# Kernel optimization log

Hardware: AMD Instinct MI355X
Metric: run time of the kernel (lower is better)

The kernel has to match this reference:

```python
import jax, jax.numpy as jnp
import numpy as np

N = 65536      # total nodes = B * MAXN
E = 524288     # edges (avg degree 8)
DX = 32; DG = 32
IN_DIM = DX + 3 * DG   # 128, after concat(x, g0, g1, g2)
H = 256; OUT = 8; MAXN = 8192


def setup_inputs() -> dict:
    key = jax.random.key(0)
    ks = jax.random.split(key, 40)
    inp = {}
    inp['x'] = jax.random.normal(ks[0], (N, DX), jnp.float32)
    inp['g0'] = jax.random.normal(ks[1], (N, DG), jnp.float32)
    inp['g1'] = jax.random.normal(ks[2], (N, DG), jnp.float32)
    inp['g2'] = jax.random.normal(ks[3], (N, DG), jnp.float32)
    inp['edge_src'] = jax.random.randint(ks[4], (E,), 0, N, jnp.int32)
    inp['edge_dst'] = jax.random.randint(ks[5], (E,), 0, N, jnp.int32)
    dims = [(IN_DIM, H), (H, H), (H, H), (H, H)]
    k = 6
    for i, (di, do) in enumerate(dims):
        s = 1.0 / np.sqrt(di)
        inp[f'Wl{i}'] = jax.random.uniform(ks[k], (di, do), jnp.float32, -s, s); k += 1
        inp[f'Wr{i}'] = jax.random.uniform(ks[k], (di, do), jnp.float32, -s, s); k += 1
        inp[f'b{i}'] = jnp.zeros((do,), jnp.float32)
    s = 1.0 / np.sqrt(MAXN)
    inp['mlp1_W1'] = jax.random.uniform(ks[k], (MAXN, H), jnp.float32, -s, s); k += 1
    inp['mlp1_b1'] = jnp.zeros((H,), jnp.float32)
    s = 1.0 / np.sqrt(H)
    inp['mlp1_W2'] = jax.random.uniform(ks[k], (H, 1), jnp.float32, -s, s); k += 1
    inp['mlp1_b2'] = jnp.zeros((1,), jnp.float32)
    inp['bn_gamma'] = jnp.ones((H,), jnp.float32)
    inp['bn_beta'] = jnp.zeros((H,), jnp.float32)
    inp['mlp2_W1'] = jax.random.uniform(ks[k], (H, H), jnp.float32, -s, s); k += 1
    inp['mlp2_b1'] = jnp.zeros((H,), jnp.float32)
    inp['mlp2_W2'] = jax.random.uniform(ks[k], (H, OUT), jnp.float32, -s, s); k += 1
    inp['mlp2_b2'] = jnp.zeros((OUT,), jnp.float32)
    return inp


def _forward(x, g0, g1, g2, edge_src, edge_dst,
             Wl0, Wr0, b0, Wl1, Wr1, b1, Wl2, Wr2, b2, Wl3, Wr3, b3,
             mlp1_W1, mlp1_b1, mlp1_W2, mlp1_b2, bn_gamma, bn_beta,
             mlp2_W1, mlp2_b1, mlp2_W2, mlp2_b2):
    h = jnp.concatenate([x, g0, g1, g2], axis=1)  # [N, IN_DIM]
    # mean-aggregation denominator (in-degree, clamped at 1 like PyG mean)
    cnt = jnp.maximum(
        jax.ops.segment_sum(jnp.ones((E,), h.dtype), edge_dst, num_segments=N), 1.0)
    for Wl, Wr, b in ((Wl0, Wr0, b0), (Wl1, Wr1, b1), (Wl2, Wr2, b2), (Wl3, Wr3, b3)):
        agg = jax.ops.segment_sum(h[edge_src], edge_dst, num_segments=N) / cnt[:, None]
        # SAGEConv: lin_l(mean of neighbors) + lin_r(self) + bias, then ReLU
        h = jax.nn.relu(agg @ Wl + h @ Wr + b)
        # F.dropout in eval / deterministic reference: identity
    h = h.reshape(-1, H, MAXN)                               # [B, H, MAXN]
    h = jax.nn.relu(jnp.einsum('bhm,mk->bhk', h, mlp1_W1) + mlp1_b1)
    h = (jnp.einsum('bhk,ko->bho', h, mlp1_W2) + mlp1_b2)[..., 0]  # [B, H]
    mean = h.mean(axis=0)
    var = h.var(axis=0)
    h = (h - mean) / jnp.sqrt(var + 1e-5) * bn_gamma + bn_beta
    h = jax.nn.relu(h)
    h = jax.nn.relu(h @ mlp2_W1 + mlp2_b1)
    return h @ mlp2_W2 + mlp2_b2                              # [B, OUT]


def reference(x, g0, g1, g2, edge_src, edge_dst,
              Wl0, Wr0, b0, Wl1, Wr1, b1, Wl2, Wr2, b2, Wl3, Wr3, b3,
              mlp1_W1, mlp1_b1, mlp1_W2, mlp1_b2, bn_gamma, bn_beta,
              mlp2_W1, mlp2_b1, mlp2_W2, mlp2_b2):
    return _forward(x, g0, g1, g2, edge_src, edge_dst,
                    Wl0, Wr0, b0, Wl1, Wr1, b1, Wl2, Wr2, b2, Wl3, Wr3, b3,
                    mlp1_W1, mlp1_b1, mlp1_W2, mlp1_b2, bn_gamma, bn_beta,
                    mlp2_W1, mlp2_b1, mlp2_W2, mlp2_b2)
```

## Files before the change

kernel.cpp:

```cpp
#include <hip/hip_runtime.h>
#include <hip/hip_bf16.h>


#define NN 65536
#define EE 524288
#define ROWS 65537
#define PCSR_CAP 983040

using frag16 = __attribute__((ext_vector_type(8))) short;
using f32x4  = __attribute__((ext_vector_type(4))) float;
using us8    = __attribute__((ext_vector_type(8))) unsigned short;
using us4v   = __attribute__((ext_vector_type(4))) unsigned short;

__device__ __forceinline__ float b2f(unsigned short u) {
    union { unsigned u32; float f; } x; x.u32 = (unsigned)u << 16; return x.f;
}

__device__ __forceinline__ void gld_lds16(const void* g, void* l) {
    __builtin_amdgcn_global_load_lds(
        (const __attribute__((address_space(1))) void*)g,
        (__attribute__((address_space(3))) void*)l, 16, 0, 0);
}

struct B1Args {
    const float* tsrc[9];
    __hip_bfloat16* tdst[9];
    int ldk[9];
    int kofs[9];
    int kblk[9];
    const float *x, *g0, *g1, *g2;
    __hip_bfloat16* h;
    int* ideg;
};

__global__ void gs_batch1(B1Args a) {
    const int z = blockIdx.z;
    const int t = threadIdx.x;
    __shared__ float tile[32][33];
    if (z == 0) {
        if (blockIdx.y != 0) return;
        int i = blockIdx.x * 256 + t;
        if (i < NN) a.ideg[i] = 0;
        return;
    }
    if (z <= 9) {
        const int m = z - 1;
        if ((int)blockIdx.x >= a.kblk[m]) return;
        const float* src = a.tsrc[m];
        __hip_bfloat16* dst = a.tdst[m];
        int ldk = a.ldk[m], kofs = a.kofs[m];
        int kb = blockIdx.x * 32, nb = blockIdx.y * 32;
        int tx = t & 31, ty = t >> 5;
#pragma unroll
        for (int i2 = 0; i2 < 32; i2 += 8)
            tile[ty + i2][tx] = src[(size_t)(kb + ty + i2) * 256 + nb + tx];
        __syncthreads();
#pragma unroll
        for (int i2 = 0; i2 < 32; i2 += 8) {
            int n = nb + ty + i2, k = kb + tx;
            dst[(size_t)n * ldk + kofs + k] = __float2bfloat16(tile[tx][ty + i2]);
        }
        return;
    }
    int vb0 = blockIdx.y * 256 + blockIdx.x;
#pragma unroll
    for (int s = 0; s < 4; ++s) {
        int idx = (s * 2048 + vb0) * 256 + t;
        int n = idx >> 5, q = idx & 31;
        int c0 = q * 4;
        const float* src = (c0 < 32) ? (a.x  + (size_t)n * 32 + c0)
                         : (c0 < 64) ? (a.g0 + (size_t)n * 32 + (c0 - 32))
                         : (c0 < 96) ? (a.g1 + (size_t)n * 32 + (c0 - 64))
                                     : (a.g2 + (size_t)n * 32 + (c0 - 96));
        f32x4 v = *(const f32x4*)src;
        union { us4v u; __hip_bfloat16 b[4]; } o;
#pragma unroll
        for (int r = 0; r < 4; ++r) o.b[r] = __float2bfloat16(v[r]);
        *(us4v*)(a.h + (size_t)n * 512 + 256 + c0) = o.u;
    }
}


__global__ void gs_hist(const int* __restrict__ dst, int* __restrict__ deg) {
    int e = blockIdx.x * 256 + threadIdx.x;
    atomicAdd(&deg[dst[e]], 1);
}

__global__ void gs_deg_reduce(const int* __restrict__ deg, int* __restrict__ bsum) {
    int t = threadIdx.x;
    int p = (deg[blockIdx.x * 256 + t] + 7) & ~7;
#pragma unroll
    for (int off = 32; off > 0; off >>= 1) p += __shfl_down(p, off);
    __shared__ int w4[4];
    if ((t & 63) == 0) w4[t >> 6] = p;
    __syncthreads();
    if (t == 0) bsum[blockIdx.x] = w4[0] + w4[1] + w4[2] + w4[3];
}

__global__ void gs_scan_apply(const int* __restrict__ deg, const int* __restrict__ bsum,
                              int* __restrict__ prow, int* __restrict__ cursor,
                              float* __restrict__ inv_cnt, int* __restrict__ pcsr,
                              __hip_bfloat16* __restrict__ P0,
                              __hip_bfloat16* __restrict__ P1) {
    __shared__ int part[256];
    int t = threadIdx.x;
    part[t] = bsum[t];
    __syncthreads();
    for (int off = 1; off < 256; off <<= 1) {
        int add = (t >= off) ? part[t - off] : 0;
        __syncthreads();
        part[t] += add;
        __syncthreads();
    }
    int blk_ofs = part[blockIdx.x] - bsum[blockIdx.x];
    int total = part[255];
    __syncthreads();
    int i = blockIdx.x * 256 + t;
    int d = deg[i];
    int p = (d + 7) & ~7;
    part[t] = p;
    __syncthreads();
    for (int off = 1; off < 256; off <<= 1) {
        int add = (t >= off) ? part[t - off] : 0;
        __syncthreads();
        part[t] += add;
        __syncthreads();
    }
    int beg = blk_ofs + part[t] - p;
    prow[i] = beg;
    cursor[i] = beg;
    inv_cnt[i] = 1.0f / (float)(d > 0 ? d : 1);
    for (int j = d; j < p; ++j) pcsr[beg + j] = NN;
    if (i == NN - 1) prow[NN] = total;
    if (blockIdx.x == 0) {
        ((unsigned*)(P0 + (size_t)NN * 512))[t] = 0u;
        ((unsigned*)(P1 + (size_t)NN * 512))[t] = 0u;
    }
}

__global__ void gs_bucket(const int* __restrict__ src, const int* __restrict__ dst,
                          int* __restrict__ cursor, int* __restrict__ pcsr) {
    int e = blockIdx.x * 256 + threadIdx.x;
    int d = dst[e];
    int p = atomicAdd(&cursor[d], 1);
    pcsr[p] = src[e];
}

template <int DIM>
__global__ void gs_agg_bf(const __hip_bfloat16* __restrict__ hsrc,
                          __hip_bfloat16* __restrict__ adst,
                          const int* __restrict__ prow, const int* __restrict__ pcsr,
                          const float* __restrict__ inv_cnt) {
    constexpr int EL = DIM / 32;
    int wave = threadIdx.x >> 6;
    int lane = threadIdx.x & 63;
    int n = blockIdx.x * 4 + wave;
    int e = prow[n], pe = prow[n + 1];
    float iv = inv_cnt[n];
    const int half = lane >> 5;
    const __hip_bfloat16* base = hsrc + (lane & 31) * EL;
    float a[EL];
#pragma unroll
    for (int k = 0; k < EL; ++k) a[k] = 0.f;
    int4 sa, sb;
    if (e < pe) { sa = *(const int4*)(pcsr + e); sb = *(const int4*)(pcsr + e + 4); }
    while (e < pe) {
        int4 ca = sa, cb = sb;
        e += 8;
        if (e < pe) { sa = *(const int4*)(pcsr + e); sb = *(const int4*)(pcsr + e + 4); }
        int r0 = half ? ca.y : ca.x;
        int r1 = half ? ca.w : ca.z;
        int r2 = half ? cb.y : cb.x;
        int r3 = half ? cb.w : cb.z;
        if constexpr (DIM == 256) {
            us8 v0 = *(const us8*)(base + (size_t)r0 * 512);
            us8 v1 = *(const us8*)(base + (size_t)r1 * 512);
            us8 v2 = *(const us8*)(base + (size_t)r2 * 512);
            us8 v3 = *(const us8*)(base + (size_t)r3 * 512);
#pragma unroll
            for (int k = 0; k < 8; ++k)
                a[k] += b2f(v0[k]) + b2f(v1[k]) + b2f(v2[k]) + b2f(v3[k]);
        } else {
            us4v v0 = *(const us4v*)(base + (size_t)r0 * 512);
            us4v v1 = *(const us4v*)(base + (size_t)r1 * 512);
            us4v v2 = *(const us4v*)(base + (size_t)r2 * 512);
            us4v v3 = *(const us4v*)(base + (size_t)r3 * 512);
#pragma unroll
            for (int k = 0; k < 4; ++k)
                a[k] += b2f(v0[k]) + b2f(v1[k]) + b2f(v2[k]) + b2f(v3[k]);
        }
    }
#pragma unroll
    for (int k = 0; k < EL; ++k) a[k] += __shfl_xor(a[k], 32);
    if (half == 0) {
        union { us8 v8; us4v v4; __hip_bfloat16 b[8]; } o;
#pragma unroll
        for (int k = 0; k < EL; ++k) o.b[k] = __float2bfloat16(a[k] * iv);
        if constexpr (DIM == 256)
            *(us8*)(adst + (size_t)n * 512 + (lane & 31) * 8) = o.v8;
        else
            *(us4v*)(adst + (size_t)n * 512 + (lane & 31) * 4) = o.v4;
    }
}


__device__ __forceinline__ void stage_tile256(const __hip_bfloat16* __restrict__ A, int lda,
                                              const __hip_bfloat16* __restrict__ Bt, int ldb,
                                              size_t row0, int kc,
                                              __hip_bfloat16* As, __hip_bfloat16* Bs) {
    const int t = threadIdx.x;
#pragma unroll
    for (int l = 0; l < 4; ++l) {
        int c = l * 512 + t;
        int row = c >> 3;
        int col = ((c & 7) ^ (row & 7)) * 8;
        gld_lds16(A + (row0 + row) * (size_t)lda + kc + col, As + c * 8);
        gld_lds16(Bt + (size_t)row * ldb + kc + col, Bs + c * 8);
    }
}

__device__ __forceinline__ void compute_tile256(const __hip_bfloat16* As,
                                                const __hip_bfloat16* Bs,
                                                int wm, int wn, int ml, int cq,
                                                f32x4 (&acc)[8][4]) {
#pragma unroll
    for (int kk = 0; kk < 2; ++kk) {
        const int g = kk * 4 + cq;
        frag16 a[8], b[4];
#pragma unroll
        for (int i = 0; i < 8; ++i) {
            int row = wm * 128 + i * 16 + ml;
            a[i] = *(const frag16*)(As + row * 64 + ((g ^ (row & 7)) * 8));
        }
#pragma unroll
        for (int j = 0; j < 4; ++j) {
            int row = wn * 64 + j * 16 + ml;
            b[j] = *(const frag16*)(Bs + row * 64 + ((g ^ (row & 7)) * 8));
        }
        __builtin_amdgcn_s_setprio(1);
#pragma unroll
        for (int i = 0; i < 8; ++i)
#pragma unroll
            for (int j = 0; j < 4; ++j)
                acc[i][j] = __builtin_amdgcn_mfma_f32_16x16x32_bf16(b[j], a[i], acc[i][j], 0, 0, 0);
        __builtin_amdgcn_s_setprio(0);
    }
}

__device__ __forceinline__ void gemm256_loop(const __hip_bfloat16* __restrict__ A, int lda,
                                             const __hip_bfloat16* __restrict__ Bt, int ldb,
                                             size_t row0, int kbeg, int nt,
                                             __hip_bfloat16 (&As)[2][256 * 64],
                                             __hip_bfloat16 (&Bs)[2][256 * 64],
                                             int wm, int wn, int ml, int cq,
                                             f32x4 (&acc)[8][4]) {
    stage_tile256(A, lda, Bt, ldb, row0, kbeg, As[0], Bs[0]);
    int cur = 0;
    for (int kt = 0; kt < nt; ++kt) {
        if (kt + 1 < nt) {
            stage_tile256(A, lda, Bt, ldb, row0, kbeg + (kt + 1) * 64, As[cur ^ 1], Bs[cur ^ 1]);
            asm volatile("s_waitcnt vmcnt(8)" ::: "memory");
        } else {
            asm volatile("s_waitcnt vmcnt(0)" ::: "memory");
        }
        asm volatile("s_barrier" ::: "memory");
        compute_tile256(As[cur], Bs[cur], wm, wn, ml, cq, acc);
        asm volatile("s_barrier" ::: "memory");
        cur ^= 1;
    }
}

__global__ __launch_bounds__(512, 2)
void gs_gemm8_bias_relu(const __hip_bfloat16* __restrict__ A, int lda, int K,
                        const __hip_bfloat16* __restrict__ Bt, int ldb,
                        const float* __restrict__ bias,
                        __hip_bfloat16* __restrict__ C, int ldc, int cofs) {
    __shared__ __hip_bfloat16 As[2][256 * 64];
    __shared__ __hip_bfloat16 Bs[2][256 * 64];
    f32x4 acc[8][4] = {};
    const size_t row0 = (size_t)blockIdx.x * 256;
    const int lane = threadIdx.x & 63, wid = threadIdx.x >> 6;
    const int wm = wid >> 2, wn = wid & 3, ml = lane & 15, cq = lane >> 4;
    gemm256_loop(A, lda, Bt, ldb, row0, 0, K / 64, As, Bs, wm, wn, ml, cq, acc);
#pragma unroll
    for (int i = 0; i < 8; ++i) {
        size_t row = row0 + wm * 128 + i * 16 + ml;
#pragma unroll
        for (int j = 0; j < 4; ++j) {
            int n0 = wn * 64 + j * 16 + cq * 4;
            f32x4 bv = *(const f32x4*)(bias + n0);
            union { us4v v; __hip_bfloat16 b[4]; } o;
#pragma unroll
            for (int r = 0; r < 4; ++r)
                o.b[r] = __float2bfloat16(fmaxf(acc[i][j][r] + bv[r], 0.f));
            *(us4v*)(C + row * (size_t)ldc + cofs + n0) = o.v;
        }
    }
}

__global__ __launch_bounds__(512, 2)
void gs_gemm8_splitk(const __hip_bfloat16* __restrict__ A, int lda,
                     const __hip_bfloat16* __restrict__ Bt, int ldb,
                     float* __restrict__ part) {
    __shared__ __hip_bfloat16 As[2][256 * 64];
    __shared__ __hip_bfloat16 Bs[2][256 * 64];
    f32x4 acc[8][4] = {};
    const size_t row0 = (size_t)blockIdx.x * 256;
    const int kbeg = blockIdx.y * 512;
    const int lane = threadIdx.x & 63, wid = threadIdx.x >> 6;
    const int wm = wid >> 2, wn = wid & 3, ml = lane & 15, cq = lane >> 4;
    gemm256_loop(A, lda, Bt, ldb, row0, kbeg, 8, As, Bs, wm, wn, ml, cq, acc);
    float* p = part + (size_t)blockIdx.y * 2048 * 256;
#pragma unroll
    for (int i = 0; i < 8; ++i) {
        size_t row = row0 + wm * 128 + i * 16 + ml;
#pragma unroll
        for (int j = 0; j < 4; ++j) {
            int n0 = wn * 64 + j * 16 + cq * 4;
            *(f32x4*)(p + row * 256 + n0) = acc[i][j];
        }
    }
}

__global__ void gs_mlp1_pool(const float* __restrict__ part, const float* __restrict__ b1,
                             const float* __restrict__ W2, const float* __restrict__ b2,
                             float* __restrict__ pooled) {
    int r = blockIdx.x;
    int t = threadIdx.x;
    float s = 0.f;
#pragma unroll
    for (int ks = 0; ks < 16; ++ks) s += part[(size_t)ks * 524288 + r * 256 + t];
    s = fmaxf(s + b1[t], 0.f) * W2[t];
#pragma unroll
    for (int off = 32; off > 0; off >>= 1) s += __shfl_down(s, off);
    __shared__ float w4[4];
    if ((t & 63) == 0) w4[t >> 6] = s;
    __syncthreads();
    if (t == 0) pooled[r] = w4[0] + w4[1] + w4[2] + w4[3] + b2[0];
}

__global__ void gs_bn_mlp2(const float* __restrict__ pooled, const float* __restrict__ gamma,
                           const float* __restrict__ beta, const float* __restrict__ W1,
                           const float* __restrict__ b1, const float* __restrict__ W2,
                           const float* __restrict__ b2, float* __restrict__ out) {
    __shared__ float hb[8][256];
    __shared__ float h2[8][256];
    int t = threadIdx.x;
    {
        float v[8];
        float m = 0.f;
#pragma unroll
        for (int b = 0; b < 8; ++b) { v[b] = pooled[b * 256 + t]; m += v[b]; }
        m *= 0.125f;
        float var = 0.f;
#pragma unroll
        for (int b = 0; b < 8; ++b) { float d = v[b] - m; var += d * d; }
        var *= 0.125f;
        float is = 1.0f / sqrtf(var + 1e-5f);
        float g = gamma[t], bt = beta[t];
#pragma unroll
        for (int b = 0; b < 8; ++b) hb[b][t] = fmaxf((v[b] - m) * is * g + bt, 0.f);
    }
    __syncthreads();
    {
        float acc[8] = {};
        for (int i = 0; i < 256; ++i) {
            float w = W1[i * 256 + t];
#pragma unroll
            for (int b = 0; b < 8; ++b) acc[b] = fmaf(hb[b][i], w, acc[b]);
        }
        float bb = b1[t];
#pragma unroll
        for (int b = 0; b < 8; ++b) h2[b][t] = fmaxf(acc[b] + bb, 0.f);
    }
    __syncthreads();
    if (t < 64) {
        int b = t >> 3, o = t & 7;
        float acc = 0.f;
        for (int j = 0; j < 256; ++j) acc = fmaf(h2[b][j], W2[j * 8 + o], acc);
        out[b * 8 + o] = acc + b2[o];
    }
}

extern "C" void kernel_launch(void* const* d_in, const int* in_sizes, int n_in,
                              void* d_out, int out_size, void* d_ws, size_t ws_size,
                              hipStream_t stream) {
    const float* x  = (const float*)d_in[0];
    const float* g0 = (const float*)d_in[1];
    const float* g1 = (const float*)d_in[2];
    const float* g2 = (const float*)d_in[3];
    const int* edge_src = (const int*)d_in[4];
    const int* edge_dst = (const int*)d_in[5];
    const float* Wl[4] = {(const float*)d_in[6], (const float*)d_in[9],
                          (const float*)d_in[12], (const float*)d_in[15]};
    const float* Wr[4] = {(const float*)d_in[7], (const float*)d_in[10],
                          (const float*)d_in[13], (const float*)d_in[16]};
    const float* bs[4] = {(const float*)d_in[8], (const float*)d_in[11],
                          (const float*)d_in[14], (const float*)d_in[17]};
    const float* mlp1_W1 = (const float*)d_in[18];
    const float* mlp1_b1 = (const float*)d_in[19];
    const float* mlp1_W2 = (const float*)d_in[20];
    const float* mlp1_b2 = (const float*)d_in[21];
    const float* bn_gamma = (const float*)d_in[22];
    const float* bn_beta  = (const float*)d_in[23];
    const float* mlp2_W1 = (const float*)d_in[24];
    const float* mlp2_b1 = (const float*)d_in[25];
    const float* mlp2_W2 = (const float*)d_in[26];
    const float* mlp2_b2 = (const float*)d_in[27];
    float* out = (float*)d_out;

    char* ws = (char*)d_ws;
    __hip_bfloat16* P0 = (__hip_bfloat16*)ws;
    __hip_bfloat16* P1 = P0 + (size_t)ROWS * 512;
    __hip_bfloat16* WC0 = P1 + (size_t)ROWS * 512;
    __hip_bfloat16* WC1 = WC0 + 65536;
    __hip_bfloat16* WC2 = WC1 + 131072;
    __hip_bfloat16* WC3 = WC2 + 131072;
    __hip_bfloat16* W1T = WC3 + 131072;
    float* inv_cnt = (float*)(W1T + 2097152);
    int* ideg = (int*)(inv_cnt + 65536);
    int* prow = ideg + 65536;
    int* cursor = prow + 65544;
    int* bsum = cursor + 65536;
    int* pcsr = bsum + 256;
    __hip_bfloat16* H4 = P0;
    float* pooled = (float*)P1 + 524288;
    float* PART = (float*)((char*)P1 + (size_t)(4 << 20));

    {
        B1Args a;
        const float* srcs[9] = {Wl[0], Wr[0], Wl[1], Wr[1], Wl[2], Wr[2], Wl[3], Wr[3],
                                mlp1_W1};
        __hip_bfloat16* dsts[9] = {WC0, WC0, WC1, WC1, WC2, WC2, WC3, WC3, W1T};
        int ldks[9] = {256, 256, 512, 512, 512, 512, 512, 512, 8192};
        int kofss[9] = {0, 128, 0, 256, 0, 256, 0, 256, 0};
        int kblks[9] = {4, 4, 8, 8, 8, 8, 8, 8, 256};
        for (int i = 0; i < 9; ++i) {
            a.tsrc[i] = srcs[i]; a.tdst[i] = dsts[i];
            a.ldk[i] = ldks[i]; a.kofs[i] = kofss[i]; a.kblk[i] = kblks[i];
        }
        a.x = x; a.g0 = g0; a.g1 = g1; a.g2 = g2;
        a.h = P0; a.ideg = ideg;
        gs_batch1<<<dim3(256, 8, 11), 256, 0, stream>>>(a);
    }

    gs_hist<<<EE / 256, 256, 0, stream>>>(edge_dst, ideg);
    gs_deg_reduce<<<256, 256, 0, stream>>>(ideg, bsum);
    gs_scan_apply<<<256, 256, 0, stream>>>(ideg, bsum, prow, cursor, inv_cnt, pcsr, P0, P1);
    gs_bucket<<<EE / 256, 256, 0, stream>>>(edge_src, edge_dst, cursor, pcsr);

    gs_agg_bf<128><<<NN / 4, 256, 0, stream>>>(P0 + 256, P0 + 128, prow, pcsr, inv_cnt);
    gs_gemm8_bias_relu<<<NN / 256, 512, 0, stream>>>(P0 + 128, 512, 256, WC0, 256,
                                                     bs[0], P1, 512, 256);
    gs_agg_bf<256><<<NN / 4, 256, 0, stream>>>(P1 + 256, P1, prow, pcsr, inv_cnt);
    gs_gemm8_bias_relu<<<NN / 256, 512, 0, stream>>>(P1, 512, 512, WC1, 512,
                                                     bs[1], P0, 512, 256);
    gs_agg_bf<256><<<NN / 4, 256, 0, stream>>>(P0 + 256, P0, prow, pcsr, inv_cnt);
    gs_gemm8_bias_relu<<<NN / 256, 512, 0, stream>>>(P0, 512, 512, WC2, 512,
                                                     bs[2], P1, 512, 256);
    gs_agg_bf<256><<<NN / 4, 256, 0, stream>>>(P1 + 256, P1, prow, pcsr, inv_cnt);
    gs_gemm8_bias_relu<<<NN / 256, 512, 0, stream>>>(P1, 512, 512, WC3, 512,
                                                     bs[3], H4, 256, 0);

    gs_gemm8_splitk<<<dim3(2048 / 256, 16), 512, 0, stream>>>(H4, 8192, W1T, 8192, PART);
    gs_mlp1_pool<<<2048, 256, 0, stream>>>(PART, mlp1_b1, mlp1_W2, mlp1_b2, pooled);

    gs_bn_mlp2<<<1, 256, 0, stream>>>(pooled, bn_gamma, bn_beta, mlp2_W1, mlp2_b1,
                                      mlp2_W2, mlp2_b2, out);
}
```

Measured before the change: 520.1 us.

## Fuse neighbor aggregation into SAGE layer GEMM kernel per 256-row tile

Merges the gather-mean aggregation kernel into the GEMM kernel: each 512-thread block first aggregates neighbor features for its own 256 rows (each wave processes 32 nodes serially), then syncs and runs the bias+ReLU GEMM on those rows. This removes four kernel launches and lets the aggregated rows be reread while possibly still in cache. In exchange, aggregation now runs with only 256 blocks at 2 blocks/CU occupancy, with long serial per-wave loops, so there is less memory-level parallelism for the random gathers than the previous 16384-block launch had. There is also no overlap between the gather phase and the MFMA phase inside a block.

```diff
diff --git a/kernel.cpp b/kernel.cpp
--- a/kernel.cpp
+++ b/kernel.cpp
@@ -144,63 +144,6 @@
     int d = dst[e];
     int p = atomicAdd(&cursor[d], 1);
     pcsr[p] = src[e];
-}
-
-template <int DIM>
-__global__ void gs_agg_bf(const __hip_bfloat16* __restrict__ hsrc,
-                          __hip_bfloat16* __restrict__ adst,
-                          const int* __restrict__ prow, const int* __restrict__ pcsr,
-                          const float* __restrict__ inv_cnt) {
-    constexpr int EL = DIM / 32;
-    int wave = threadIdx.x >> 6;
-    int lane = threadIdx.x & 63;
-    int n = blockIdx.x * 4 + wave;
-    int e = prow[n], pe = prow[n + 1];
-    float iv = inv_cnt[n];
-    const int half = lane >> 5;
-    const __hip_bfloat16* base = hsrc + (lane & 31) * EL;
-    float a[EL];
-#pragma unroll
-    for (int k = 0; k < EL; ++k) a[k] = 0.f;
-    int4 sa, sb;
-    if (e < pe) { sa = *(const int4*)(pcsr + e); sb = *(const int4*)(pcsr + e + 4); }
-    while (e < pe) {
-        int4 ca = sa, cb = sb;
-        e += 8;
-        if (e < pe) { sa = *(const int4*)(pcsr + e); sb = *(const int4*)(pcsr + e + 4); }
-        int r0 = half ? ca.y : ca.x;
-        int r1 = half ? ca.w : ca.z;
-        int r2 = half ? cb.y : cb.x;
-        int r3 = half ? cb.w : cb.z;
-        if constexpr (DIM == 256) {
-            us8 v0 = *(const us8*)(base + (size_t)r0 * 512);
-            us8 v1 = *(const us8*)(base + (size_t)r1 * 512);
-            us8 v2 = *(const us8*)(base + (size_t)r2 * 512);
-            us8 v3 = *(const us8*)(base + (size_t)r3 * 512);
-#pragma unroll
-            for (int k = 0; k < 8; ++k)
-                a[k] += b2f(v0[k]) + b2f(v1[k]) + b2f(v2[k]) + b2f(v3[k]);
-        } else {
-            us4v v0 = *(const us4v*)(base + (size_t)r0 * 512);
-            us4v v1 = *(const us4v*)(base + (size_t)r1 * 512);
-            us4v v2 = *(const us4v*)(base + (size_t)r2 * 512);
-            us4v v3 = *(const us4v*)(base + (size_t)r3 * 512);
-#pragma unroll
-            for (int k = 0; k < 4; ++k)
-                a[k] += b2f(v0[k]) + b2f(v1[k]) + b2f(v2[k]) + b2f(v3[k]);
-        }
-    }
-#pragma unroll
-    for (int k = 0; k < EL; ++k) a[k] += __shfl_xor(a[k], 32);
-    if (half == 0) {
-        union { us8 v8; us4v v4; __hip_bfloat16 b[8]; } o;
-#pragma unroll
-        for (int k = 0; k < EL; ++k) o.b[k] = __float2bfloat16(a[k] * iv);
-        if constexpr (DIM == 256)
-            *(us8*)(adst + (size_t)n * 512 + (lane & 31) * 8) = o.v8;
-        else
-            *(us4v*)(adst + (size_t)n * 512 + (lane & 31) * 4) = o.v4;
-    }
 }
 
 
@@ -270,16 +213,78 @@
     }
 }
 
+template <int DIM>
 __global__ __launch_bounds__(512, 2)
-void gs_gemm8_bias_relu(const __hip_bfloat16* __restrict__ A, int lda, int K,
-                        const __hip_bfloat16* __restrict__ Bt, int ldb,
-                        const float* __restrict__ bias,
-                        __hip_bfloat16* __restrict__ C, int ldc, int cofs) {
+void gs_sage_layer(const __hip_bfloat16* __restrict__ hsrc,
+                   __hip_bfloat16* __restrict__ adst,
+                   const int* __restrict__ prow, const int* __restrict__ pcsr,
+                   const float* __restrict__ inv_cnt,
+                   const __hip_bfloat16* __restrict__ A, int lda, int K,
+                   const __hip_bfloat16* __restrict__ Bt, int ldb,
+                   const float* __restrict__ bias,
+                   __hip_bfloat16* __restrict__ C, int ldc, int cofs) {
     __shared__ __hip_bfloat16 As[2][256 * 64];
     __shared__ __hip_bfloat16 Bs[2][256 * 64];
+    const int lane = threadIdx.x & 63, wid = threadIdx.x >> 6;
+
+    {
+        constexpr int EL = DIM / 32;
+        const int half = lane >> 5;
+        const __hip_bfloat16* base = hsrc + (lane & 31) * EL;
+        const int n0 = blockIdx.x * 256 + wid * 32;
+        for (int u = 0; u < 32; ++u) {
+            int n = n0 + u;
+            int e = prow[n], pe = prow[n + 1];
+            float iv = inv_cnt[n];
+            float a[EL];
+#pragma unroll
+            for (int k = 0; k < EL; ++k) a[k] = 0.f;
+            int4 sa, sb;
+            if (e < pe) { sa = *(const int4*)(pcsr + e); sb = *(const int4*)(pcsr + e + 4); }
+            while (e < pe) {
+                int4 ca = sa, cb = sb;
+                e += 8;
+                if (e < pe) { sa = *(const int4*)(pcsr + e); sb = *(const int4*)(pcsr + e + 4); }
+                int r0 = half ? ca.y : ca.x;
+                int r1 = half ? ca.w : ca.z;
+                int r2 = half ? cb.y : cb.x;
+                int r3 = half ? cb.w : cb.z;
+                if constexpr (DIM == 256) {
+                    us8 v0 = *(const us8*)(base + (size_t)r0 * 512);
+                    us8 v1 = *(const us8*)(base + (size_t)r1 * 512);
+                    us8 v2 = *(const us8*)(base + (size_t)r2 * 512);
+                    us8 v3 = *(const us8*)(base + (size_t)r3 * 512);
+#pragma unroll
+                    for (int k = 0; k < 8; ++k)
+                        a[k] += b2f(v0[k]) + b2f(v1[k]) + b2f(v2[k]) + b2f(v3[k]);
+                } else {
+                    us4v v0 = *(const us4v*)(base + (size_t)r0 * 512);
+                    us4v v1 = *(const us4v*)(base + (size_t)r1 * 512);
+                    us4v v2 = *(const us4v*)(base + (size_t)r2 * 512);
+                    us4v v3 = *(const us4v*)(base + (size_t)r3 * 512);
+#pragma unroll
+                    for (int k = 0; k < 4; ++k)
+                        a[k] += b2f(v0[k]) + b2f(v1[k]) + b2f(v2[k]) + b2f(v3[k]);
+                }
+            }
+#pragma unroll
+            for (int k = 0; k < EL; ++k) a[k] += __shfl_xor(a[k], 32);
+            if (half == 0) {
+                union { us8 v8; us4v v4; __hip_bfloat16 b[8]; } o;
+#pragma unroll
+                for (int k = 0; k < EL; ++k) o.b[k] = __float2bfloat16(a[k] * iv);
+                if constexpr (DIM == 256)
+                    *(us8*)(adst + (size_t)n * 512 + (lane & 31) * 8) = o.v8;
+                else
+                    *(us4v*)(adst + (size_t)n * 512 + (lane & 31) * 4) = o.v4;
+            }
+        }
+    }
+    asm volatile("s_waitcnt vmcnt(0)" ::: "memory");
+    __syncthreads();
+
     f32x4 acc[8][4] = {};
     const size_t row0 = (size_t)blockIdx.x * 256;
-    const int lane = threadIdx.x & 63, wid = threadIdx.x >> 6;
     const int wm = wid >> 2, wn = wid & 3, ml = lane & 15, cq = lane >> 4;
     gemm256_loop(A, lda, Bt, ldb, row0, 0, K / 64, As, Bs, wm, wn, ml, cq, acc);
 #pragma unroll
@@ -449,18 +454,18 @@
     gs_scan_apply<<<256, 256, 0, stream>>>(ideg, bsum, prow, cursor, inv_cnt, pcsr, P0, P1);
     gs_bucket<<<EE / 256, 256, 0, stream>>>(edge_src, edge_dst, cursor, pcsr);
 
-    gs_agg_bf<128><<<NN / 4, 256, 0, stream>>>(P0 + 256, P0 + 128, prow, pcsr, inv_cnt);
-    gs_gemm8_bias_relu<<<NN / 256, 512, 0, stream>>>(P0 + 128, 512, 256, WC0, 256,
-                                                     bs[0], P1, 512, 256);
-    gs_agg_bf<256><<<NN / 4, 256, 0, stream>>>(P1 + 256, P1, prow, pcsr, inv_cnt);
-    gs_gemm8_bias_relu<<<NN / 256, 512, 0, stream>>>(P1, 512, 512, WC1, 512,
-                                                     bs[1], P0, 512, 256);
-    gs_agg_bf<256><<<NN / 4, 256, 0, stream>>>(P0 + 256, P0, prow, pcsr, inv_cnt);
-    gs_gemm8_bias_relu<<<NN / 256, 512, 0, stream>>>(P0, 512, 512, WC2, 512,
-                                                     bs[2], P1, 512, 256);
-    gs_agg_bf<256><<<NN / 4, 256, 0, stream>>>(P1 + 256, P1, prow, pcsr, inv_cnt);
-    gs_gemm8_bias_relu<<<NN / 256, 512, 0, stream>>>(P1, 512, 512, WC3, 512,
-                                                     bs[3], H4, 256, 0);
+    gs_sage_layer<128><<<NN / 256, 512, 0, stream>>>(
+        P0 + 256, P0 + 128, prow, pcsr, inv_cnt,
+        P0 + 128, 512, 256, WC0, 256, bs[0], P1, 512, 256);
+    gs_sage_layer<256><<<NN / 256, 512, 0, stream>>>(
+        P1 + 256, P1, prow, pcsr, inv_cnt,
+        P1, 512, 512, WC1, 512, bs[1], P0, 512, 256);
+    gs_sage_layer<256><<<NN / 256, 512, 0, stream>>>(
+        P0 + 256, P0, prow, pcsr, inv_cnt,
+        P0, 512, 512, WC2, 512, bs[2], P1, 512, 256);
+    gs_sage_layer<256><<<NN / 256, 512, 0, stream>>>(
+        P1 + 256, P1, prow, pcsr, inv_cnt,
+        P1, 512, 512, WC3, 512, bs[3], H4, 256, 0);
 
     gs_gemm8_splitk<<<dim3(2048 / 256, 16), 512, 0, stream>>>(H4, 8192, W1T, 8192, PART);
     gs_mlp1_pool<<<2048, 256, 0, stream>>>(PART, mlp1_b1, mlp1_W2, mlp1_b2, pooled);
```

After: 564.2 us. 8.5% more time.

## Pad CSR rows to 4 and use full-wave gathers in aggregation

Applied to the files above, without the earlier changes.

The neighbour padding granularity in the CSR drops from 8 to 4, so there are fewer dummy padding edges. The aggregation kernel changes from split half-waves, each handling half the neighbours with wider loads, to a full 64-lane wave that covers the whole feature row with narrower per-lane loads, processing 4 neighbours per iteration. This removes the cross-half shuffle reduction and the gathers wasted on padding, but each lane now issues narrower memory requests.

```diff
diff --git a/kernel.cpp b/kernel.cpp
--- a/kernel.cpp
+++ b/kernel.cpp
@@ -5,11 +5,10 @@
 #define NN 65536
 #define EE 524288
 #define ROWS 65537
-#define PCSR_CAP 983040
+#define PCSR_CAP 720896
 
 using frag16 = __attribute__((ext_vector_type(8))) short;
 using f32x4  = __attribute__((ext_vector_type(4))) float;
-using us8    = __attribute__((ext_vector_type(8))) unsigned short;
 using us4v   = __attribute__((ext_vector_type(4))) unsigned short;
 
 __device__ __forceinline__ float b2f(unsigned short u) {
@@ -88,7 +87,7 @@
 
 __global__ void gs_deg_reduce(const int* __restrict__ deg, int* __restrict__ bsum) {
     int t = threadIdx.x;
-    int p = (deg[blockIdx.x * 256 + t] + 7) & ~7;
+    int p = (deg[blockIdx.x * 256 + t] + 3) & ~3;
 #pragma unroll
     for (int off = 32; off > 0; off >>= 1) p += __shfl_down(p, off);
     __shared__ int w4[4];
@@ -117,7 +116,7 @@
     __syncthreads();
     int i = blockIdx.x * 256 + t;
     int d = deg[i];
-    int p = (d + 7) & ~7;
+    int p = (d + 3) & ~3;
     part[t] = p;
     __syncthreads();
     for (int off = 1; off < 256; off <<= 1) {
@@ -151,55 +150,52 @@
                           __hip_bfloat16* __restrict__ adst,
                           const int* __restrict__ prow, const int* __restrict__ pcsr,
                           const float* __restrict__ inv_cnt) {
-    constexpr int EL = DIM / 32;
     int wave = threadIdx.x >> 6;
     int lane = threadIdx.x & 63;
     int n = blockIdx.x * 4 + wave;
     int e = prow[n], pe = prow[n + 1];
     float iv = inv_cnt[n];
-    const int half = lane >> 5;
-    const __hip_bfloat16* base = hsrc + (lane & 31) * EL;
-    float a[EL];
-#pragma unroll
-    for (int k = 0; k < EL; ++k) a[k] = 0.f;
-    int4 sa, sb;
-    if (e < pe) { sa = *(const int4*)(pcsr + e); sb = *(const int4*)(pcsr + e + 4); }
-    while (e < pe) {
-        int4 ca = sa, cb = sb;
-        e += 8;
-        if (e < pe) { sa = *(const int4*)(pcsr + e); sb = *(const int4*)(pcsr + e + 4); }
-        int r0 = half ? ca.y : ca.x;
-        int r1 = half ? ca.w : ca.z;
-        int r2 = half ? cb.y : cb.x;
-        int r3 = half ? cb.w : cb.z;
-        if constexpr (DIM == 256) {
-            us8 v0 = *(const us8*)(base + (size_t)r0 * 512);
-            us8 v1 = *(const us8*)(base + (size_t)r1 * 512);
-            us8 v2 = *(const us8*)(base + (size_t)r2 * 512);
-            us8 v3 = *(const us8*)(base + (size_t)r3 * 512);
-#pragma unroll
-            for (int k = 0; k < 8; ++k)
-                a[k] += b2f(v0[k]) + b2f(v1[k]) + b2f(v2[k]) + b2f(v3[k]);
-        } else {
-            us4v v0 = *(const us4v*)(base + (size_t)r0 * 512);
-            us4v v1 = *(const us4v*)(base + (size_t)r1 * 512);
-            us4v v2 = *(const us4v*)(base + (size_t)r2 * 512);
-            us4v v3 = *(const us4v*)(base + (size_t)r3 * 512);
-#pragma unroll
-            for (int k = 0; k < 4; ++k)
-                a[k] += b2f(v0[k]) + b2f(v1[k]) + b2f(v2[k]) + b2f(v3[k]);
-        }
-    }
-#pragma unroll
-    for (int k = 0; k < EL; ++k) a[k] += __shfl_xor(a[k], 32);
-    if (half == 0) {
-        union { us8 v8; us4v v4; __hip_bfloat16 b[8]; } o;
-#pragma unroll
-        for (int k = 0; k < EL; ++k) o.b[k] = __float2bfloat16(a[k] * iv);
-        if constexpr (DIM == 256)
-            *(us8*)(adst + (size_t)n * 512 + (lane & 31) * 8) = o.v8;
-        else
-            *(us4v*)(adst + (size_t)n * 512 + (lane & 31) * 4) = o.v4;
+    if constexpr (DIM == 256) {
+        const __hip_bfloat16* base = hsrc + lane * 4;
+        float a0 = 0.f, a1 = 0.f, a2 = 0.f, a3 = 0.f;
+        int4 s4;
+        if (e < pe) s4 = *(const int4*)(pcsr + e);
+        while (e < pe) {
+            int4 cur = s4;
+            e += 4;
+            if (e < pe) s4 = *(const int4*)(pcsr + e);
+            ushort4 v0 = *(const ushort4*)(base + (size_t)cur.x * 512);
+            ushort4 v1 = *(const ushort4*)(base + (size_t)cur.y * 512);
+            ushort4 v2 = *(const ushort4*)(base + (size_t)cur.z * 512);
+            ushort4 v3 = *(const ushort4*)(base + (size_t)cur.w * 512);
+            a0 += b2f(v0.x); a1 += b2f(v0.y); a2 += b2f(v0.z); a3 += b2f(v0.w);
+            a0 += b2f(v1.x); a1 += b2f(v1.y); a2 += b2f(v1.z); a3 += b2f(v1.w);
+            a0 += b2f(v2.x); a1 += b2f(v2.y); a2 += b2f(v2.z); a3 += b2f(v2.w);
+            a0 += b2f(v3.x); a1 += b2f(v3.y); a2 += b2f(v3.z); a3 += b2f(v3.w);
+        }
+        __hip_bfloat16 o[4] = {__float2bfloat16(a0 * iv), __float2bfloat16(a1 * iv),
+                               __float2bfloat16(a2 * iv), __float2bfloat16(a3 * iv)};
+        *(ushort4*)(adst + (size_t)n * 512 + lane * 4) = *(const ushort4*)o;
+    } else {
+        const __hip_bfloat16* base = hsrc + lane * 2;
+        float a0 = 0.f, a1 = 0.f;
+        int4 s4;
+        if (e < pe) s4 = *(const int4*)(pcsr + e);
+        while (e < pe) {
+            int4 cur = s4;
+            e += 4;
+            if (e < pe) s4 = *(const int4*)(pcsr + e);
+            ushort2 v0 = *(const ushort2*)(base + (size_t)cur.x * 512);
+            ushort2 v1 = *(const ushort2*)(base + (size_t)cur.y * 512);
+            ushort2 v2 = *(const ushort2*)(base + (size_t)cur.z * 512);
+            ushort2 v3 = *(const ushort2*)(base + (size_t)cur.w * 512);
+            a0 += b2f(v0.x); a1 += b2f(v0.y);
+            a0 += b2f(v1.x); a1 += b2f(v1.y);
+            a0 += b2f(v2.x); a1 += b2f(v2.y);
+            a0 += b2f(v3.x); a1 += b2f(v3.y);
+        }
+        __hip_bfloat16 o[2] = {__float2bfloat16(a0 * iv), __float2bfloat16(a1 * iv)};
+        *(ushort2*)(adst + (size_t)n * 512 + lane * 2) = *(const ushort2*)o;
     }
 }
 
```

Measured after the change: 524.6 us. About the same (+0.9%).
